# Kernel optimization log

Hardware: AMD Instinct MI355X
Metric: run time of the kernel (lower is better)

## Reference

```python
import jax, jax.numpy as jnp
import numpy as np
import math

B, N, H, HEADS = 2, 4096, 256, 4
DH = H // HEADS
SCALE = math.sqrt(DH)


def setup_inputs() -> dict:
    key = jax.random.key(0)
    ks = jax.random.split(key, 8)
    h = jax.random.normal(ks[0], (B, N, H), dtype=jnp.float32)
    tau = jax.random.uniform(ks[1], (B, N), dtype=jnp.float32)  # trust scores in [0,1]
    adj_mask = jax.random.randint(ks[2], (N, N), 0, 2, dtype=jnp.int32)
    s = 0.02
    Wq = jax.random.normal(ks[3], (H, H), dtype=jnp.float32) * s
    Wk = jax.random.normal(ks[4], (H, H), dtype=jnp.float32) * s
    Wv = jax.random.normal(ks[5], (H, H), dtype=jnp.float32) * s
    Wo = jax.random.normal(ks[6], (H, H), dtype=jnp.float32) * s
    cw = jax.random.normal(ks[7], (HEADS,), dtype=jnp.float32) * s  # credibility_proj weight (num_heads,1) squeezed
    bq = jnp.zeros((H,), jnp.float32)
    bk = jnp.zeros((H,), jnp.float32)
    bv = jnp.zeros((H,), jnp.float32)
    bo = jnp.zeros((H,), jnp.float32)
    cb = jnp.zeros((HEADS,), jnp.float32)
    return {"h": h, "tau": tau, "adj_mask": adj_mask,
            "Wq": Wq, "bq": bq, "Wk": Wk, "bk": bk, "Wv": Wv, "bv": bv,
            "cw": cw, "cb": cb, "Wo": Wo, "bo": bo}


def reference(h, tau, adj_mask, Wq, bq, Wk, bk, Wv, bv, cw, cb, Wo, bo):
    # QKV projections -> (B, heads, N, head_dim)
    def proj(x, W, b):
        y = jnp.einsum('bnh,oh->bno', x, W) + b
        return y.reshape(B, N, HEADS, DH).transpose(0, 2, 1, 3)

    Q = proj(h, Wq, bq)
    K = proj(h, Wk, bk)
    V = proj(h, Wv, bv)

    scores = jnp.einsum('bhnd,bhmd->bhnm', Q, K) / SCALE  # (B,heads,N,N)
    # credibility bias: Linear(1 -> heads) applied to tau_i * tau_j
    tt = tau[:, :, None] * tau[:, None, :]                 # (B,N,N)
    cred = tt[:, None, :, :] * cw[None, :, None, None] + cb[None, :, None, None]
    scores = scores + cred
    # adjacency mask
    scores = jnp.where(adj_mask[None, None, :, :] == 0, -jnp.inf, scores)
    attention = jax.nn.softmax(scores, axis=-1)
    # dropout is identity in eval mode
    h_out = jnp.einsum('bhnm,bhmd->bhnd', attention, V)
    h_out = h_out.transpose(0, 2, 1, 3).reshape(B, N, H)
    h_out = jnp.einsum('bnh,oh->bno', h_out, Wo) + bo
    return h_out, attention.mean(axis=1)
```

## Files before the change

### kernel.cpp

```cpp
#include <hip/hip_runtime.h>

#define B_ 2
#define N_ 4096
#define H_ 256
#define HEADS_ 4
#define DH_ 64

typedef _Float16 f16;
typedef f16 f16x8 __attribute__((ext_vector_type(8)));
typedef f16 f16x4 __attribute__((ext_vector_type(4)));
typedef float f32x4 __attribute__((ext_vector_type(4)));


#define HOUT_OFF 2097152

__global__ __launch_bounds__(256) void cvt_kernel(
    const float* __restrict__ h, const float* __restrict__ Wq,
    const float* __restrict__ Wk, const float* __restrict__ Wv,
    const float* __restrict__ Wo, f16* __restrict__ ws) {
  int i = blockIdx.x * 256 + threadIdx.x;
  const int NH = 2097152;
  if (i < NH) {
    ws[i] = (f16)h[i];
  } else if (i < NH + 4 * 65536) {
    int j = i - NH;
    int sel = j >> 16;
    int k = j & 65535;
    const float* src = sel == 0 ? Wq : sel == 1 ? Wk : sel == 2 ? Wv : Wo;
    ws[i] = (f16)src[k];
  }
}

__global__ __launch_bounds__(256) void pack_adj_kernel(
    const int* __restrict__ adj, unsigned long long* __restrict__ adjb) {
  int g = blockIdx.x * 256 + threadIdx.x;
  int lane = threadIdx.x & 63;
  int av = adj[g] != 0;
  unsigned long long m = __ballot(av);
  if (lane == 0) adjb[g >> 6] = m;
}

__global__ __launch_bounds__(256) void proj_kernel(
    const f16* __restrict__ hh, const f16* __restrict__ Wh,
    const float* __restrict__ bq, const float* __restrict__ bk,
    const float* __restrict__ bv, f16* __restrict__ Qh, f16* __restrict__ Kf,
    f16* __restrict__ Vf) {
  const int tid = threadIdx.x;
  const int lane = tid & 63, w = tid >> 6;
  const int q = lane >> 4, c = lane & 15;
  const int wsel = blockIdx.y >> 2, head = blockIdx.y & 3;
  const int m0 = blockIdx.x * 64 + w * 16;
  const f16* W = Wh + wsel * 65536;
  const int o0 = head * 64;

  f32x4 acc[4] = {};
  for (int k0 = 0; k0 < 256; k0 += 32) {
    f16x8 a = *(const f16x8*)(hh + (size_t)(m0 + c) * 256 + k0 + q * 8);
#pragma unroll
    for (int cg = 0; cg < 4; ++cg) {
      f16x8 bfr = *(const f16x8*)(W + (size_t)(o0 + cg * 16 + c) * 256 + k0 + q * 8);
      acc[cg] = __builtin_amdgcn_mfma_f32_16x16x32_f16(a, bfr, acc[cg], 0, 0, 0);
    }
  }
  const int b = m0 >> 12, n = m0 & 4095;
  const int bh2 = b * HEADS_ + head;
  if (wsel == 2) {
    const int jt = n >> 6;
    f16* vbase = Vf + (((size_t)bh2 * 64 + jt) * 8) * 512;
#pragma unroll
    for (int cg = 0; cg < 4; ++cg) {
      float bb = bv[o0 + cg * 16 + c];
#pragma unroll
      for (int r = 0; r < 4; ++r) {
        int jj = w * 16 + q * 4 + r;
        vbase[(size_t)(((jj >> 5) * 4 + cg) * 512) + ((jj >> 3) & 3) * 128 +
              c * 8 + (jj & 7)] = (f16)(acc[cg][r] + bb);
      }
    }
  } else if (wsel == 1) {
    const int t = n >> 4;
    f16* kbase = Kf + (((size_t)bh2 * 256 + t) * 2) * 512;
#pragma unroll
    for (int cg = 0; cg < 4; ++cg) {
      float bb = bk[o0 + cg * 16 + c];
      const int half = cg >> 1;
      const int qf = ((cg & 1) * 16 + c) >> 3;
      f16* kb2 = kbase + half * 512 + qf * 128 + (c & 7);
#pragma unroll
      for (int r = 0; r < 4; ++r) kb2[(q * 4 + r) * 8] = (f16)(acc[cg][r] + bb);
    }
  } else {
#pragma unroll
    for (int cg = 0; cg < 4; ++cg) {
      int dh = cg * 16 + c;
      float bb = bq[o0 + dh];
#pragma unroll
      for (int r = 0; r < 4; ++r)
        Qh[((size_t)bh2 * N_ + n + q * 4 + r) * DH_ + dh] =
            (f16)((acc[cg][r] + bb) * 0.125f);
    }
  }
}

#define TS 68
#define WTILE (16 * TS)

__global__ __launch_bounds__(256, 1) void attn_sum_kernel(
    const f16* __restrict__ Qh, const f16* __restrict__ Kf,
    const f16* __restrict__ Vf, const float* __restrict__ tau,
    const uint2* __restrict__ adjb, const float* __restrict__ cw,
    f16* __restrict__ Oh, float* __restrict__ rsum_ws) {
  __shared__ float lds[4 * WTILE];
  __shared__ float lred[4][64];
  const int gid = blockIdx.x;
  const int bh = gid & 7;
  const int b = bh >> 2, h = bh & 3;
  const int i0 = (gid >> 3) * 64;
  const int tid = threadIdx.x;
  const int lane = tid & 63, jq = tid >> 6;
  const int q = lane >> 4, c = lane & 15;

  f16x8 a0[4], a1[4];
  float tau_i[4][4];
#pragma unroll
  for (int ig = 0; ig < 4; ++ig) {
    const f16* Qbase = Qh + ((size_t)bh * N_ + i0 + ig * 16 + c) * DH_;
    a0[ig] = *(const f16x8*)(Qbase + q * 8);
    a1[ig] = *(const f16x8*)(Qbase + 32 + q * 8);
#pragma unroll
    for (int r = 0; r < 4; ++r)
      tau_i[ig][r] = tau[b * N_ + i0 + ig * 16 + q * 4 + r];
  }
  const float cw_h = cw[h];
  const f16* Kfb = Kf + (size_t)bh * 262144 + lane * 8;
  const f16* Vfb = Vf + (size_t)bh * 262144 + lane * 8;
  const float* taub = tau + b * N_;
  const int jbase = jq * 1024;

  float lsum[4][4] = {};
  f32x4 oacc[4][4] = {};
  float* myp = lds + jq * WTILE;

#pragma unroll 1
  for (int it = 0; it < 16; ++it) {
    const int j0 = jbase + it * 64;
    f16x8 kf[8], vf[8];
    {
      const f16* kt = Kfb + (size_t)(j0 >> 4) * 1024;
#pragma unroll
      for (int f = 0; f < 8; ++f) kf[f] = *(const f16x8*)(kt + f * 512);
    }
    {
      const f16* vt = Vfb + (size_t)(j0 >> 6) * 4096;
#pragma unroll
      for (int f = 0; f < 8; ++f) vf[f] = *(const f16x8*)(vt + f * 512);
    }
    float tj[4];
#pragma unroll
    for (int cg = 0; cg < 4; ++cg) tj[cg] = taub[j0 + cg * 16 + c];

#pragma unroll
    for (int ig = 0; ig < 4; ++ig) {
      uint2 aw[4];
#pragma unroll
      for (int r = 0; r < 4; ++r)
        aw[r] = adjb[(size_t)(i0 + ig * 16 + q * 4 + r) * 64 + (j0 >> 6)];
#pragma unroll
      for (int cg = 0; cg < 4; ++cg) {
        f32x4 s = {};
        s = __builtin_amdgcn_mfma_f32_16x16x32_f16(a0[ig], kf[2 * cg], s, 0, 0, 0);
        s = __builtin_amdgcn_mfma_f32_16x16x32_f16(a1[ig], kf[2 * cg + 1], s, 0, 0, 0);
        const float credj = cw_h * tj[cg];
        const unsigned shift = (cg & 1) * 16 + c;
#pragma unroll
        for (int r = 0; r < 4; ++r) {
          unsigned mword = (cg < 2) ? aw[r].x : aw[r].y;
          float e = __expf(s[r] + credj * tau_i[ig][r]);
          e = ((mword >> shift) & 1) ? e : 0.f;
          lsum[ig][r] += e;
          myp[(q * 4 + r) * TS + cg * 16 + c] = e;
        }
      }
#pragma unroll
      for (int ks = 0; ks < 2; ++ks) {
        f32x4 plo = *(f32x4*)(myp + c * TS + ks * 32 + q * 8);
        f32x4 phi = *(f32x4*)(myp + c * TS + ks * 32 + q * 8 + 4);
        f16x8 pa;
#pragma unroll
        for (int t = 0; t < 4; ++t) {
          pa[t] = (f16)plo[t];
          pa[4 + t] = (f16)phi[t];
        }
#pragma unroll
        for (int cg = 0; cg < 4; ++cg)
          oacc[ig][cg] = __builtin_amdgcn_mfma_f32_16x16x32_f16(
              pa, vf[ks * 4 + cg], oacc[ig][cg], 0, 0, 0);
      }
    }
  }

#pragma unroll
  for (int ig = 0; ig < 4; ++ig) {
#pragma unroll
    for (int r = 0; r < 4; ++r) {
      float v = lsum[ig][r];
      v += __shfl_xor(v, 1);
      v += __shfl_xor(v, 2);
      v += __shfl_xor(v, 4);
      v += __shfl_xor(v, 8);
      lsum[ig][r] = v;
    }
  }
  if (c == 0) {
#pragma unroll
    for (int ig = 0; ig < 4; ++ig)
#pragma unroll
      for (int r = 0; r < 4; ++r) lred[jq][ig * 16 + q * 4 + r] = lsum[ig][r];
  }
  __syncthreads();

#pragma unroll
  for (int ig = 0; ig < 4; ++ig) {
    float linv[4];
#pragma unroll
    for (int r = 0; r < 4; ++r) {
      int row = ig * 16 + q * 4 + r;
      linv[r] = 1.0f / (lred[0][row] + lred[1][row] + lred[2][row] +
                        lred[3][row]);
    }
    if (jq == 0 && c == 0) {
#pragma unroll
      for (int r = 0; r < 4; ++r)
        rsum_ws[bh * N_ + i0 + ig * 16 + q * 4 + r] = linv[r];
    }
    if (jq != 0) {
#pragma unroll
      for (int cg = 0; cg < 4; ++cg)
#pragma unroll
        for (int r = 0; r < 4; ++r) myp[(cg * 4 + r) * 64 + lane] = oacc[ig][cg][r];
    }
    __syncthreads();
    if (jq == 0) {
#pragma unroll
      for (int cg = 0; cg < 4; ++cg)
#pragma unroll
        for (int r = 0; r < 4; ++r) {
          float v = oacc[ig][cg][r];
#pragma unroll
          for (int jj = 1; jj < 4; ++jj)
            v += lds[jj * WTILE + (cg * 4 + r) * 64 + lane];
          Oh[((size_t)(b * N_) + i0 + ig * 16 + q * 4 + r) * H_ + h * 64 +
             cg * 16 + c] = (f16)(v * linv[r]);
        }
    }
    __syncthreads();
  }
}

__global__ __launch_bounds__(256, 1) void attn_mean_kernel(
    const f16* __restrict__ Qh, const f16* __restrict__ Kf,
    const float* __restrict__ tau, const uint2* __restrict__ adjb,
    const float* __restrict__ cw, const float* __restrict__ linv_ws,
    float* __restrict__ out) {
  const int gid = blockIdx.x;
  const int b = gid & 1;
  const int jq = (gid >> 1) & 3;
  const int i0 = (gid >> 3) * 32;
  const int tid = threadIdx.x;
  const int lane = tid & 63, w = tid >> 6;
  const int q = lane >> 4, c = lane & 15;

  float li[4][2][4];
  float cwh[4];
#pragma unroll
  for (int h = 0; h < 4; ++h) {
    cwh[h] = cw[h];
#pragma unroll
    for (int ig = 0; ig < 2; ++ig)
#pragma unroll
      for (int r = 0; r < 4; ++r)
        li[h][ig][r] =
            linv_ws[(b * 4 + h) * N_ + i0 + ig * 16 + q * 4 + r] * 0.25f;
  }
  float tau_i[2][4];
#pragma unroll
  for (int ig = 0; ig < 2; ++ig)
#pragma unroll
    for (int r = 0; r < 4; ++r)
      tau_i[ig][r] = tau[b * N_ + i0 + ig * 16 + q * 4 + r];
  const float* taub = tau + b * N_;

#pragma unroll 1
  for (int it = 0; it < 4; ++it) {
    const int j0 = jq * 1024 + (it * 4 + w) * 64;
    uint2 aw[2][4];
#pragma unroll
    for (int ig = 0; ig < 2; ++ig)
#pragma unroll
      for (int r = 0; r < 4; ++r)
        aw[ig][r] = adjb[(size_t)(i0 + ig * 16 + q * 4 + r) * 64 + (j0 >> 6)];
    float tj[4];
#pragma unroll
    for (int cg = 0; cg < 4; ++cg) tj[cg] = taub[j0 + cg * 16 + c];

    f32x4 macc[2][4] = {};
#pragma unroll
    for (int h = 0; h < 4; ++h) {
      f16x8 kf[8];
      {
        const f16* kt = Kf + (size_t)(b * 4 + h) * 262144 +
                        (size_t)(j0 >> 4) * 1024 + lane * 8;
#pragma unroll
        for (int f = 0; f < 8; ++f) kf[f] = *(const f16x8*)(kt + f * 512);
      }
#pragma unroll
      for (int ig = 0; ig < 2; ++ig) {
        const f16* Qbase =
            Qh + ((size_t)(b * 4 + h) * N_ + i0 + ig * 16 + c) * DH_;
        f16x8 a0 = *(const f16x8*)(Qbase + q * 8);
        f16x8 a1 = *(const f16x8*)(Qbase + 32 + q * 8);
#pragma unroll
        for (int cg = 0; cg < 4; ++cg) {
          f32x4 s = {};
          s = __builtin_amdgcn_mfma_f32_16x16x32_f16(a0, kf[2 * cg], s, 0, 0, 0);
          s = __builtin_amdgcn_mfma_f32_16x16x32_f16(a1, kf[2 * cg + 1], s, 0, 0, 0);
          const float credj = cwh[h] * tj[cg];
          const unsigned shift = (cg & 1) * 16 + c;
#pragma unroll
          for (int r = 0; r < 4; ++r) {
            unsigned mword = (cg < 2) ? aw[ig][r].x : aw[ig][r].y;
            float e = __expf(s[r] + credj * tau_i[ig][r]);
            float lw = ((mword >> shift) & 1) ? li[h][ig][r] : 0.f;
            macc[ig][cg][r] += e * lw;
          }
        }
      }
    }
#pragma unroll
    for (int ig = 0; ig < 2; ++ig)
#pragma unroll
      for (int cg = 0; cg < 4; ++cg)
#pragma unroll
        for (int r = 0; r < 4; ++r)
          out[((size_t)(b * N_) + i0 + ig * 16 + q * 4 + r) * N_ + j0 +
              cg * 16 + c] = macc[ig][cg][r];
  }
}

__global__ __launch_bounds__(256) void oproj_kernel(
    const f16* __restrict__ Oh, const f16* __restrict__ Woh,
    const float* __restrict__ bo, float* __restrict__ out) {
  const int tid = threadIdx.x, lane = tid & 63, w = tid >> 6;
  const int q = lane >> 4, c = lane & 15;
  const int m0 = blockIdx.x * 64 + w * 16;
  const int o0 = blockIdx.y * 64;
  f32x4 acc[4] = {};
  for (int k0 = 0; k0 < 256; k0 += 32) {
    f16x8 a = *(const f16x8*)(Oh + (size_t)(m0 + c) * 256 + k0 + q * 8);
#pragma unroll
    for (int cg = 0; cg < 4; ++cg) {
      f16x8 bfr = *(const f16x8*)(Woh + (size_t)(o0 + cg * 16 + c) * 256 + k0 + q * 8);
      acc[cg] = __builtin_amdgcn_mfma_f32_16x16x32_f16(a, bfr, acc[cg], 0, 0, 0);
    }
  }
#pragma unroll
  for (int cg = 0; cg < 4; ++cg) {
    float bb = bo[o0 + cg * 16 + c];
#pragma unroll
    for (int r = 0; r < 4; ++r)
      out[(size_t)(m0 + q * 4 + r) * 256 + o0 + cg * 16 + c] = acc[cg][r] + bb;
  }
}

extern "C" void kernel_launch(void* const* d_in, const int* in_sizes, int n_in,
                              void* d_out, int out_size, void* d_ws,
                              size_t ws_size, hipStream_t stream) {
  const float* h   = (const float*)d_in[0];
  const float* tau = (const float*)d_in[1];
  const int*   adj = (const int*)d_in[2];
  const float* Wq  = (const float*)d_in[3];
  const float* bq  = (const float*)d_in[4];
  const float* Wk  = (const float*)d_in[5];
  const float* bk  = (const float*)d_in[6];
  const float* Wv  = (const float*)d_in[7];
  const float* bv  = (const float*)d_in[8];
  const float* cw  = (const float*)d_in[9];
  const float* Wo  = (const float*)d_in[11];
  const float* bo  = (const float*)d_in[12];
  float* out = (float*)d_out;

  f16* ws   = (f16*)d_ws;
  f16* h_h  = ws;
  f16* W_h  = ws + 2097152;
  f16* Wo_h = W_h + 3 * 65536;
  f16* Q_h  = ws + 2359296;
  f16* K_f  = ws + 4456448;
  f16* V_f  = ws + 6553600;
  f16* O_h  = ws + 8650752;
  unsigned long long* adjb = (unsigned long long*)(ws + 10747904);
  float* rsum_ws = (float*)ws;

  pack_adj_kernel<<<dim3(65536), dim3(256), 0, stream>>>(adj, adjb);
  cvt_kernel<<<dim3(9216), dim3(256), 0, stream>>>(h, Wq, Wk, Wv, Wo, ws);
  proj_kernel<<<dim3(128, 12), dim3(256), 0, stream>>>(h_h, W_h, bq, bk, bv, Q_h,
                                                       K_f, V_f);
  attn_sum_kernel<<<dim3(512), dim3(256), 0, stream>>>(
      Q_h, K_f, V_f, tau, (const uint2*)adjb, cw, O_h, rsum_ws);
  attn_mean_kernel<<<dim3(1024), dim3(256), 0, stream>>>(
      Q_h, K_f, tau, (const uint2*)adjb, cw, rsum_ws, out + HOUT_OFF);
  oproj_kernel<<<dim3(128, 4), dim3(256), 0, stream>>>(O_h, Wo_h, bo, out);
}
```

Measured before the change: 405.8 us.

## Halve attention-sum row tile and double-buffer K/Q loads in mean kernel

The attention-sum kernel now handles 32 query rows per block instead of 64 and launches 1024 blocks, giving the GPU more parallelism. Each of the two row groups gets its own LDS probability tile, so both score passes run before the PV MFMAs, and the V load is moved after the first pass. The attention-mean kernel double-buffers the K fragments and Q operands across heads, prefetching the next head's data while computing the current one. In exchange, K tiles are re-read by twice as many blocks and the prefetch buffers raise register pressure.

```diff
diff --git a/kernel.cpp b/kernel.cpp
--- a/kernel.cpp
+++ b/kernel.cpp
@@ -110,20 +110,20 @@
     const f16* __restrict__ Vf, const float* __restrict__ tau,
     const uint2* __restrict__ adjb, const float* __restrict__ cw,
     f16* __restrict__ Oh, float* __restrict__ rsum_ws) {
-  __shared__ float lds[4 * WTILE];
-  __shared__ float lred[4][64];
+  __shared__ float lds[8 * WTILE];
+  __shared__ float lred[4][32];
   const int gid = blockIdx.x;
   const int bh = gid & 7;
   const int b = bh >> 2, h = bh & 3;
-  const int i0 = (gid >> 3) * 64;
+  const int i0 = (gid >> 3) * 32;
   const int tid = threadIdx.x;
   const int lane = tid & 63, jq = tid >> 6;
   const int q = lane >> 4, c = lane & 15;
 
-  f16x8 a0[4], a1[4];
-  float tau_i[4][4];
-#pragma unroll
-  for (int ig = 0; ig < 4; ++ig) {
+  f16x8 a0[2], a1[2];
+  float tau_i[2][4];
+#pragma unroll
+  for (int ig = 0; ig < 2; ++ig) {
     const f16* Qbase = Qh + ((size_t)bh * N_ + i0 + ig * 16 + c) * DH_;
     a0[ig] = *(const f16x8*)(Qbase + q * 8);
     a1[ig] = *(const f16x8*)(Qbase + 32 + q * 8);
@@ -137,50 +137,77 @@
   const float* taub = tau + b * N_;
   const int jbase = jq * 1024;
 
-  float lsum[4][4] = {};
-  f32x4 oacc[4][4] = {};
-  float* myp = lds + jq * WTILE;
+  float lsum[2][4] = {};
+  f32x4 oacc[2][4] = {};
+  float* myp0 = lds + (jq * 2) * WTILE;
+  float* myp1 = myp0 + WTILE;
 
 #pragma unroll 1
   for (int it = 0; it < 16; ++it) {
     const int j0 = jbase + it * 64;
-    f16x8 kf[8], vf[8];
+    f16x8 kf[8];
     {
       const f16* kt = Kfb + (size_t)(j0 >> 4) * 1024;
 #pragma unroll
       for (int f = 0; f < 8; ++f) kf[f] = *(const f16x8*)(kt + f * 512);
     }
+    float tj[4];
+#pragma unroll
+    for (int cg = 0; cg < 4; ++cg) tj[cg] = taub[j0 + cg * 16 + c];
+
+    {
+      uint2 aw[4];
+#pragma unroll
+      for (int r = 0; r < 4; ++r)
+        aw[r] = adjb[(size_t)(i0 + q * 4 + r) * 64 + (j0 >> 6)];
+#pragma unroll
+      for (int cg = 0; cg < 4; ++cg) {
+        f32x4 s = {};
+        s = __builtin_amdgcn_mfma_f32_16x16x32_f16(a0[0], kf[2 * cg], s, 0, 0, 0);
+        s = __builtin_amdgcn_mfma_f32_16x16x32_f16(a1[0], kf[2 * cg + 1], s, 0, 0, 0);
+        const float credj = cw_h * tj[cg];
+        const unsigned shift = (cg & 1) * 16 + c;
+#pragma unroll
+        for (int r = 0; r < 4; ++r) {
+          unsigned mword = (cg < 2) ? aw[r].x : aw[r].y;
+          float e = __expf(s[r] + credj * tau_i[0][r]);
+          e = ((mword >> shift) & 1) ? e : 0.f;
+          lsum[0][r] += e;
+          myp0[(q * 4 + r) * TS + cg * 16 + c] = e;
+        }
+      }
+    }
+    f16x8 vf[8];
     {
       const f16* vt = Vfb + (size_t)(j0 >> 6) * 4096;
 #pragma unroll
       for (int f = 0; f < 8; ++f) vf[f] = *(const f16x8*)(vt + f * 512);
     }
-    float tj[4];
-#pragma unroll
-    for (int cg = 0; cg < 4; ++cg) tj[cg] = taub[j0 + cg * 16 + c];
-
-#pragma unroll
-    for (int ig = 0; ig < 4; ++ig) {
+    {
       uint2 aw[4];
 #pragma unroll
       for (int r = 0; r < 4; ++r)
-        aw[r] = adjb[(size_t)(i0 + ig * 16 + q * 4 + r) * 64 + (j0 >> 6)];
+        aw[r] = adjb[(size_t)(i0 + 16 + q * 4 + r) * 64 + (j0 >> 6)];
 #pragma unroll
       for (int cg = 0; cg < 4; ++cg) {
         f32x4 s = {};
-        s = __builtin_amdgcn_mfma_f32_16x16x32_f16(a0[ig], kf[2 * cg], s, 0, 0, 0);
-        s = __builtin_amdgcn_mfma_f32_16x16x32_f16(a1[ig], kf[2 * cg + 1], s, 0, 0, 0);
+        s = __builtin_amdgcn_mfma_f32_16x16x32_f16(a0[1], kf[2 * cg], s, 0, 0, 0);
+        s = __builtin_amdgcn_mfma_f32_16x16x32_f16(a1[1], kf[2 * cg + 1], s, 0, 0, 0);
         const float credj = cw_h * tj[cg];
         const unsigned shift = (cg & 1) * 16 + c;
 #pragma unroll
         for (int r = 0; r < 4; ++r) {
           unsigned mword = (cg < 2) ? aw[r].x : aw[r].y;
-          float e = __expf(s[r] + credj * tau_i[ig][r]);
+          float e = __expf(s[r] + credj * tau_i[1][r]);
           e = ((mword >> shift) & 1) ? e : 0.f;
-          lsum[ig][r] += e;
-          myp[(q * 4 + r) * TS + cg * 16 + c] = e;
-        }
-      }
+          lsum[1][r] += e;
+          myp1[(q * 4 + r) * TS + cg * 16 + c] = e;
+        }
+      }
+    }
+#pragma unroll
+    for (int ig = 0; ig < 2; ++ig) {
+      float* myp = ig ? myp1 : myp0;
 #pragma unroll
       for (int ks = 0; ks < 2; ++ks) {
         f32x4 plo = *(f32x4*)(myp + c * TS + ks * 32 + q * 8);
@@ -200,7 +227,7 @@
   }
 
 #pragma unroll
-  for (int ig = 0; ig < 4; ++ig) {
+  for (int ig = 0; ig < 2; ++ig) {
 #pragma unroll
     for (int r = 0; r < 4; ++r) {
       float v = lsum[ig][r];
@@ -213,14 +240,14 @@
   }
   if (c == 0) {
 #pragma unroll
-    for (int ig = 0; ig < 4; ++ig)
+    for (int ig = 0; ig < 2; ++ig)
 #pragma unroll
       for (int r = 0; r < 4; ++r) lred[jq][ig * 16 + q * 4 + r] = lsum[ig][r];
   }
   __syncthreads();
 
 #pragma unroll
-  for (int ig = 0; ig < 4; ++ig) {
+  for (int ig = 0; ig < 2; ++ig) {
     float linv[4];
 #pragma unroll
     for (int r = 0; r < 4; ++r) {
@@ -237,7 +264,7 @@
 #pragma unroll
       for (int cg = 0; cg < 4; ++cg)
 #pragma unroll
-        for (int r = 0; r < 4; ++r) myp[(cg * 4 + r) * 64 + lane] = oacc[ig][cg][r];
+        for (int r = 0; r < 4; ++r) myp0[(cg * 4 + r) * 64 + lane] = oacc[ig][cg][r];
     }
     __syncthreads();
     if (jq == 0) {
@@ -248,7 +275,7 @@
           float v = oacc[ig][cg][r];
 #pragma unroll
           for (int jj = 1; jj < 4; ++jj)
-            v += lds[jj * WTILE + (cg * 4 + r) * 64 + lane];
+            v += lds[(jj * 2) * WTILE + (cg * 4 + r) * 64 + lane];
           Oh[((size_t)(b * N_) + i0 + ig * 16 + q * 4 + r) * H_ + h * 64 +
              cg * 16 + c] = (f16)(v * linv[r]);
         }
@@ -289,6 +316,22 @@
     for (int r = 0; r < 4; ++r)
       tau_i[ig][r] = tau[b * N_ + i0 + ig * 16 + q * 4 + r];
   const float* taub = tau + b * N_;
+  const f16* KfB = Kf + (size_t)(b * 4) * 262144 + lane * 8;
+  const f16* QB = Qh + ((size_t)(b * 4) * N_ + i0 + c) * DH_;
+
+  f16x8 kf2[2][8];
+  f16x8 qa[2][2][2];
+  {
+    const int j0 = jq * 1024 + (0 * 4 + w) * 64;
+    const f16* kt = KfB + (size_t)(j0 >> 4) * 1024;
+#pragma unroll
+    for (int f = 0; f < 8; ++f) kf2[0][f] = *(const f16x8*)(kt + f * 512);
+#pragma unroll
+    for (int ig = 0; ig < 2; ++ig) {
+      qa[0][ig][0] = *(const f16x8*)(QB + ig * 1024 + q * 8);
+      qa[0][ig][1] = *(const f16x8*)(QB + ig * 1024 + 32 + q * 8);
+    }
+  }
 
 #pragma unroll 1
   for (int it = 0; it < 4; ++it) {
@@ -306,24 +349,30 @@
     f32x4 macc[2][4] = {};
 #pragma unroll
     for (int h = 0; h < 4; ++h) {
-      f16x8 kf[8];
+      const int cur = h & 1, nx = cur ^ 1;
       {
-        const f16* kt = Kf + (size_t)(b * 4 + h) * 262144 +
-                        (size_t)(j0 >> 4) * 1024 + lane * 8;
-#pragma unroll
-        for (int f = 0; f < 8; ++f) kf[f] = *(const f16x8*)(kt + f * 512);
+        const int hn = (h + 1) & 3;
+        const int itn = (h < 3) ? it : (it < 3 ? it + 1 : it);
+        const int j0n = jq * 1024 + (itn * 4 + w) * 64;
+        const f16* ktn = KfB + (size_t)hn * 262144 + (size_t)(j0n >> 4) * 1024;
+#pragma unroll
+        for (int f = 0; f < 8; ++f) kf2[nx][f] = *(const f16x8*)(ktn + f * 512);
+        const f16* qn = QB + (size_t)hn * 262144;
+#pragma unroll
+        for (int ig = 0; ig < 2; ++ig) {
+          qa[nx][ig][0] = *(const f16x8*)(qn + ig * 1024 + q * 8);
+          qa[nx][ig][1] = *(const f16x8*)(qn + ig * 1024 + 32 + q * 8);
+        }
       }
 #pragma unroll
       for (int ig = 0; ig < 2; ++ig) {
-        const f16* Qbase =
-            Qh + ((size_t)(b * 4 + h) * N_ + i0 + ig * 16 + c) * DH_;
-        f16x8 a0 = *(const f16x8*)(Qbase + q * 8);
-        f16x8 a1 = *(const f16x8*)(Qbase + 32 + q * 8);
 #pragma unroll
         for (int cg = 0; cg < 4; ++cg) {
           f32x4 s = {};
-          s = __builtin_amdgcn_mfma_f32_16x16x32_f16(a0, kf[2 * cg], s, 0, 0, 0);
-          s = __builtin_amdgcn_mfma_f32_16x16x32_f16(a1, kf[2 * cg + 1], s, 0, 0, 0);
+          s = __builtin_amdgcn_mfma_f32_16x16x32_f16(qa[cur][ig][0],
+                                                     kf2[cur][2 * cg], s, 0, 0, 0);
+          s = __builtin_amdgcn_mfma_f32_16x16x32_f16(
+              qa[cur][ig][1], kf2[cur][2 * cg + 1], s, 0, 0, 0);
           const float credj = cwh[h] * tj[cg];
           const unsigned shift = (cg & 1) * 16 + c;
 #pragma unroll
@@ -404,7 +453,7 @@
   cvt_kernel<<<dim3(9216), dim3(256), 0, stream>>>(h, Wq, Wk, Wv, Wo, ws);
   proj_kernel<<<dim3(128, 12), dim3(256), 0, stream>>>(h_h, W_h, bq, bk, bv, Q_h,
                                                        K_f, V_f);
-  attn_sum_kernel<<<dim3(512), dim3(256), 0, stream>>>(
+  attn_sum_kernel<<<dim3(1024), dim3(256), 0, stream>>>(
       Q_h, K_f, V_f, tau, (const uint2*)adjb, cw, O_h, rsum_ws);
   attn_mean_kernel<<<dim3(1024), dim3(256), 0, stream>>>(
       Q_h, K_f, tau, (const uint2*)adjb, cw, rsum_ws, out + HOUT_OFF);
```

Measured after the change: 414.2 us. 1.02x slower.
